# Optimization experiments

Measured on AMD Instinct MI355X. Metric: run time of the kernel, lower is better.

The kernel has to match this reference:

```python
import jax, jax.numpy as jnp
import numpy as np

B, S, E, H = 32, 2048, 256, 256

def setup_inputs() -> dict:
    key = jax.random.key(0)
    ks = jax.random.split(key, 8)
    scale = 1.0 / np.sqrt(H)  # kaiming-uniform-ish magnitude
    return {
        "x": jax.random.normal(ks[0], (B, S, E), dtype=jnp.float32),
        "h0": jax.random.normal(ks[1], (B, H), dtype=jnp.float32),
        "Wz": jax.random.normal(ks[2], (E, H), dtype=jnp.float32) * scale,
        "Uz": jax.random.normal(ks[3], (H, H), dtype=jnp.float32) * scale,
        "Wr": jax.random.normal(ks[4], (E, H), dtype=jnp.float32) * scale,
        "Ur": jax.random.normal(ks[5], (H, H), dtype=jnp.float32) * scale,
        "Wh": jax.random.normal(ks[6], (E, H), dtype=jnp.float32) * scale,
        "Uh": jax.random.normal(ks[7], (H, H), dtype=jnp.float32) * scale,
    }

def reference(x, h0, Wz, Uz, Wr, Ur, Wh, Uh):
    # Precompute input-side projections for all timesteps in three big GEMMs,
    # then scan the recurrence over time. Math identical to the per-step loop.
    xz = jnp.einsum('bse,eh->sbh', x, Wz)  # [S,B,H]
    xr = jnp.einsum('bse,eh->sbh', x, Wr)
    xh = jnp.einsum('bse,eh->sbh', x, Wh)

    def step(h, inp):
        xz_t, xr_t, xh_t = inp
        z = jax.nn.sigmoid(xz_t + h @ Uz)
        r = jax.nn.sigmoid(xr_t + h @ Ur)
        h_wave = jnp.tanh(xh_t + (r * h) @ Uh)
        h_new = (1.0 - z) * h + z * h_wave
        return h_new, h_new

    _, Ht = jax.lax.scan(step, h0, (xz, xr, xh))  # Ht: [S,B,H]
    return jnp.transpose(Ht, (1, 0, 2))  # [B,S,H]
```

## Files before the change

kernel.cpp:

```cpp
#include <hip/hip_runtime.h>

typedef _Float16 f16;
typedef _Float16 f16x2 __attribute__((ext_vector_type(2)));
typedef _Float16 f16x8 __attribute__((ext_vector_type(8)));
typedef __fp16   h16x2 __attribute__((ext_vector_type(2)));
typedef float    f32x4 __attribute__((ext_vector_type(4)));

#define B_ 32
#define S_ 2048
#define E_ 256
#define H_ 256
#define M_ (B_ * S_)

union U32F2 { unsigned int u; f16x2 h; h16x2 g; };

__device__ __forceinline__ float fdot2f(f16x2 a, f16x2 b, float c) {
#if __has_builtin(__builtin_amdgcn_fdot2)
  return __builtin_amdgcn_fdot2(a, b, c, false);
#else
  return c + (float)a.x * (float)b.x + (float)a.y * (float)b.y;
#endif
}

__device__ __forceinline__ float fast_exp2(float x) {
#if __has_builtin(__builtin_amdgcn_exp2f)
  return __builtin_amdgcn_exp2f(x);
#else
  return exp2f(x);
#endif
}
__device__ __forceinline__ float fast_rcp(float x) {
#if __has_builtin(__builtin_amdgcn_rcpf)
  return __builtin_amdgcn_rcpf(x);
#else
  return 1.0f / x;
#endif
}

__device__ __forceinline__ float sigm(float x) {
  float e = fast_exp2(-1.4426950408889634f * x);
  return fast_rcp(1.0f + e);
}
__device__ __forceinline__ float tanh_fast(float x) {
  x = fminf(15.0f, fmaxf(-15.0f, x));
  float e = fast_exp2(2.8853900817779268f * x);
  return (e - 1.0f) * fast_rcp(e + 1.0f);
}

__global__ __launch_bounds__(256, 4) void proj_gemm(
    const float* __restrict__ x, const float* __restrict__ Wz,
    const float* __restrict__ Wr, const float* __restrict__ Wh,
    f16* __restrict__ Xg) {
  __shared__ __align__(16) f16 Wl[64][264];
  const int tid = threadIdx.x;
  const int wv = tid >> 6;
  const int ln = tid & 63;
  const int M0 = blockIdx.x * 64;
  const int nb = blockIdx.y;
  const int gate = nb >> 2;
  const int c0 = (nb & 3) * 64;
  const float* W = (gate == 0) ? Wz : (gate == 1 ? Wr : Wh);

#pragma unroll
  for (int i = 0; i < 64; ++i) {
    int e = i * 256 + tid;
    int cl = e & 63;
    int k = e >> 6;
    Wl[cl][k] = (f16)W[(size_t)k * H_ + c0 + cl];
  }
  __syncthreads();

  const int row = M0 + wv * 16 + (ln & 15);
  const int kg = (ln >> 4) * 8;
  f32x4 acc0 = {0.f, 0.f, 0.f, 0.f};
  f32x4 acc1 = {0.f, 0.f, 0.f, 0.f};
  f32x4 acc2 = {0.f, 0.f, 0.f, 0.f};
  f32x4 acc3 = {0.f, 0.f, 0.f, 0.f};

#pragma unroll
  for (int kk = 0; kk < 8; ++kk) {
    const int k0 = kk * 32;
    const float* ap = x + (size_t)row * E_ + k0 + kg;
    float4 a0 = *(const float4*)ap;
    float4 a1 = *(const float4*)(ap + 4);
    f16x8 af = {(f16)a0.x, (f16)a0.y, (f16)a0.z, (f16)a0.w,
                (f16)a1.x, (f16)a1.y, (f16)a1.z, (f16)a1.w};
    f16x8 b0 = *(const f16x8*)&Wl[0 * 16 + (ln & 15)][k0 + kg];
    f16x8 b1 = *(const f16x8*)&Wl[1 * 16 + (ln & 15)][k0 + kg];
    f16x8 b2 = *(const f16x8*)&Wl[2 * 16 + (ln & 15)][k0 + kg];
    f16x8 b3 = *(const f16x8*)&Wl[3 * 16 + (ln & 15)][k0 + kg];
    acc0 = __builtin_amdgcn_mfma_f32_16x16x32_f16(af, b0, acc0, 0, 0, 0);
    acc1 = __builtin_amdgcn_mfma_f32_16x16x32_f16(af, b1, acc1, 0, 0, 0);
    acc2 = __builtin_amdgcn_mfma_f32_16x16x32_f16(af, b2, acc2, 0, 0, 0);
    acc3 = __builtin_amdgcn_mfma_f32_16x16x32_f16(af, b3, acc3, 0, 0, 0);
  }

  f16* outg = Xg + (size_t)gate * ((size_t)M_ * H_);
  const int rbase = M0 + wv * 16 + (ln >> 4) * 4;
#define EPI(NT, ACC)                                                       \
  {                                                                        \
    const int cc = c0 + NT * 16 + (ln & 15);                               \
    outg[(size_t)(rbase + 0) * H_ + cc] = (f16)ACC[0];                     \
    outg[(size_t)(rbase + 1) * H_ + cc] = (f16)ACC[1];                     \
    outg[(size_t)(rbase + 2) * H_ + cc] = (f16)ACC[2];                     \
    outg[(size_t)(rbase + 3) * H_ + cc] = (f16)ACC[3];                     \
  }
  EPI(0, acc0) EPI(1, acc1) EPI(2, acc2) EPI(3, acc3)
#undef EPI
}

__global__ __launch_bounds__(512, 2) void gru_rec(
    const f16* __restrict__ Xg, const float* __restrict__ h0,
    const float* __restrict__ Uz, const float* __restrict__ Ur,
    const float* __restrict__ Uh, float* __restrict__ out) {
  __shared__ uint4 h2v[32];
  __shared__ uint4 rh2v[32];
  const int b = blockIdx.x;
  const int tid = threadIdx.x;
  const int wv = tid >> 6;
  const int ln = tid & 63;
  const int c = wv * 32 + (ln & 31);
  const int hi = ln >> 5;
  const bool owner = (hi == 0);

  f16x2 wz[64], wr[64], wh[64];
  {
    const int rb = hi * 128;
#pragma unroll
    for (int j = 0; j < 64; ++j) {
      const size_t o0 = (size_t)(rb + 2 * j) * H_ + c;
      const size_t o1 = o0 + H_;
      wz[j] = f16x2{(f16)Uz[o0], (f16)Uz[o1]};
      wr[j] = f16x2{(f16)Ur[o0], (f16)Ur[o1]};
      wh[j] = f16x2{(f16)Uh[o0], (f16)Uh[o1]};
    }
  }

  float h_reg = 0.f;
  if (owner) h_reg = h0[b * H_ + c];
  {
    float hn = __shfl_xor(h_reg, 1);
    if (owner && !(ln & 1)) {
      U32F2 p; p.g = __builtin_amdgcn_cvt_pkrtz(h_reg, hn);
      ((unsigned int*)h2v)[c >> 1] = p.u;
    }
  }
  __syncthreads();

  const f16* xz = Xg + (size_t)b * ((size_t)S_ * H_) + c;
  const f16* xr = xz + (size_t)M_ * H_;
  const f16* xh = xr + (size_t)M_ * H_;
  float* outp = out + (size_t)b * ((size_t)S_ * H_) + c;

  f16 pz = xz[0], pr = xr[0], ph = xh[0];

  for (int t = 0; t < S_; ++t) {
    const float xzc = (float)pz, xrc = (float)pr, xhc = (float)ph;
    {
      const int t2 = (t + 1 < S_) ? (t + 1) : t;
      const size_t off = (size_t)t2 * H_;
      pz = xz[off]; pr = xr[off]; ph = xh[off];
    }

    float az = 0.f, ar = 0.f;
#pragma unroll
    for (int q = 0; q < 16; ++q) {
      uint4 hv = h2v[hi * 16 + q];
      U32F2 p0, p1, p2, p3;
      p0.u = hv.x; p1.u = hv.y; p2.u = hv.z; p3.u = hv.w;
      az = fdot2f(wz[4 * q + 0], p0.h, az);
      az = fdot2f(wz[4 * q + 1], p1.h, az);
      az = fdot2f(wz[4 * q + 2], p2.h, az);
      az = fdot2f(wz[4 * q + 3], p3.h, az);
      ar = fdot2f(wr[4 * q + 0], p0.h, ar);
      ar = fdot2f(wr[4 * q + 1], p1.h, ar);
      ar = fdot2f(wr[4 * q + 2], p2.h, ar);
      ar = fdot2f(wr[4 * q + 3], p3.h, ar);
    }
    az += __shfl_xor(az, 32);
    ar += __shfl_xor(ar, 32);

    float z_s = 0.f, rh = 0.f;
    if (owner) {
      z_s = sigm(az + xzc);
      float rr = sigm(ar + xrc);
      rh = rr * h_reg;
    }
    {
      float rhn = __shfl_xor(rh, 1);
      if (owner && !(ln & 1)) {
        U32F2 p; p.g = __builtin_amdgcn_cvt_pkrtz(rh, rhn);
        ((unsigned int*)rh2v)[c >> 1] = p.u;
      }
    }
    __syncthreads();

    float ah = 0.f;
#pragma unroll
    for (int q = 0; q < 16; ++q) {
      uint4 rv = rh2v[hi * 16 + q];
      U32F2 p0, p1, p2, p3;
      p0.u = rv.x; p1.u = rv.y; p2.u = rv.z; p3.u = rv.w;
      ah = fdot2f(wh[4 * q + 0], p0.h, ah);
      ah = fdot2f(wh[4 * q + 1], p1.h, ah);
      ah = fdot2f(wh[4 * q + 2], p2.h, ah);
      ah = fdot2f(wh[4 * q + 3], p3.h, ah);
    }
    ah += __shfl_xor(ah, 32);

    if (owner) {
      float ht = tanh_fast(ah + xhc);
      h_reg = h_reg + z_s * (ht - h_reg);
      outp[(size_t)t * H_] = h_reg;
    }
    {
      float hn = __shfl_xor(h_reg, 1);
      if (owner && !(ln & 1)) {
        U32F2 p; p.g = __builtin_amdgcn_cvt_pkrtz(h_reg, hn);
        ((unsigned int*)h2v)[c >> 1] = p.u;
      }
    }
    __syncthreads();
  }
}

extern "C" void kernel_launch(void* const* d_in, const int* in_sizes, int n_in,
                              void* d_out, int out_size, void* d_ws,
                              size_t ws_size, hipStream_t stream) {
  const float* x  = (const float*)d_in[0];
  const float* h0 = (const float*)d_in[1];
  const float* Wz = (const float*)d_in[2];
  const float* Uz = (const float*)d_in[3];
  const float* Wr = (const float*)d_in[4];
  const float* Ur = (const float*)d_in[5];
  const float* Wh = (const float*)d_in[6];
  const float* Uh = (const float*)d_in[7];
  float* out = (float*)d_out;

  const size_t need = (size_t)3 * M_ * H_ * sizeof(f16);
  if (ws_size < need) return;
  f16* Xg = (f16*)d_ws;

  proj_gemm<<<dim3(M_ / 64, 12), 256, 0, stream>>>(x, Wz, Wr, Wh, Xg);
  gru_rec<<<dim3(B_), 512, 0, stream>>>(Xg, h0, Uz, Ur, Uh, out);
}
```

Baseline: 2.967 ms.

## Split GRU recurrence K-dimension four ways across 1024-thread blocks

The recurrent kernel now uses 1024 threads per batch row. Each column's 256-long dot product is split across four 16-lane groups instead of two 32-lane halves, which halves the serial fdot2 chain per step and the weight registers per thread. The shared hidden-state vectors are padded per quarter so the four groups read from different banks. The Uh dot product is split into two accumulators for more ILP. In exchange, each step pays an extra cross-lane reduction, and each barrier now synchronises 16 waves instead of 8.

After: 3.633 ms. +22.4%, slower.

```diff
diff --git a/kernel.cpp b/kernel.cpp
--- a/kernel.cpp
+++ b/kernel.cpp
@@ -21,6 +21,10 @@
   return c + (float)a.x * (float)b.x + (float)a.y * (float)b.y;
 #endif
 }
+__device__ __forceinline__ float fdot2u(unsigned int w, unsigned int v, float c) {
+  U32F2 a, b; a.u = w; b.u = v;
+  return fdot2f(a.h, b.h, c);
+}
 
 __device__ __forceinline__ float fast_exp2(float x) {
 #if __has_builtin(__builtin_amdgcn_exp2f)
@@ -36,7 +40,6 @@
   return 1.0f / x;
 #endif
 }
-
 __device__ __forceinline__ float sigm(float x) {
   float e = fast_exp2(-1.4426950408889634f * x);
   return fast_rcp(1.0f + e);
@@ -109,31 +112,38 @@
 #undef EPI
 }
 
-__global__ __launch_bounds__(512, 2) void gru_rec(
+__global__ __launch_bounds__(1024) void gru_rec(
     const f16* __restrict__ Xg, const float* __restrict__ h0,
     const float* __restrict__ Uz, const float* __restrict__ Ur,
     const float* __restrict__ Uh, float* __restrict__ out) {
-  __shared__ uint4 h2v[32];
-  __shared__ uint4 rh2v[32];
+  __shared__ __align__(16) unsigned int h2v[4 * 36];
+  __shared__ __align__(16) unsigned int rh2v[4 * 36];
   const int b = blockIdx.x;
   const int tid = threadIdx.x;
   const int wv = tid >> 6;
   const int ln = tid & 63;
-  const int c = wv * 32 + (ln & 31);
-  const int hi = ln >> 5;
-  const bool owner = (hi == 0);
-
-  f16x2 wz[64], wr[64], wh[64];
+  const int c = wv * 16 + (ln & 15);
+  const int kq = ln >> 4;
+  const bool owner = (kq == 0);
+
+  unsigned int wzU[32], wrU[32], whU[32];
   {
-    const int rb = hi * 128;
-#pragma unroll
-    for (int j = 0; j < 64; ++j) {
+    const int rb = kq * 64;
+#pragma unroll
+    for (int j = 0; j < 32; ++j) {
       const size_t o0 = (size_t)(rb + 2 * j) * H_ + c;
-      const size_t o1 = o0 + H_;
-      wz[j] = f16x2{(f16)Uz[o0], (f16)Uz[o1]};
-      wr[j] = f16x2{(f16)Ur[o0], (f16)Ur[o1]};
-      wh[j] = f16x2{(f16)Uh[o0], (f16)Uh[o1]};
-    }
+      U32F2 pz, pr, ph;
+      pz.h = f16x2{(f16)Uz[o0], (f16)Uz[o0 + H_]};
+      pr.h = f16x2{(f16)Ur[o0], (f16)Ur[o0 + H_]};
+      ph.h = f16x2{(f16)Uh[o0], (f16)Uh[o0 + H_]};
+      wzU[j] = pz.u; wrU[j] = pr.u; whU[j] = ph.u;
+    }
+  }
+#pragma unroll
+  for (int j = 0; j < 32; ++j) {
+    asm("" : "+v"(wzU[j]));
+    asm("" : "+v"(wrU[j]));
+    asm("" : "+v"(whU[j]));
   }
 
   float h_reg = 0.f;
@@ -142,7 +152,8 @@
     float hn = __shfl_xor(h_reg, 1);
     if (owner && !(ln & 1)) {
       U32F2 p; p.g = __builtin_amdgcn_cvt_pkrtz(h_reg, hn);
-      ((unsigned int*)h2v)[c >> 1] = p.u;
+      const int pi = c >> 1;
+      h2v[(pi >> 5) * 36 + (pi & 31)] = p.u;
     }
   }
   __syncthreads();
@@ -153,6 +164,9 @@
   float* outp = out + (size_t)b * ((size_t)S_ * H_) + c;
 
   f16 pz = xz[0], pr = xr[0], ph = xh[0];
+
+  const uint4* hq = (const uint4*)(h2v + kq * 36);
+  const uint4* rq = (const uint4*)(rh2v + kq * 36);
 
   for (int t = 0; t < S_; ++t) {
     const float xzc = (float)pz, xrc = (float)pr, xhc = (float)ph;
@@ -164,21 +178,19 @@
 
     float az = 0.f, ar = 0.f;
 #pragma unroll
-    for (int q = 0; q < 16; ++q) {
-      uint4 hv = h2v[hi * 16 + q];
-      U32F2 p0, p1, p2, p3;
-      p0.u = hv.x; p1.u = hv.y; p2.u = hv.z; p3.u = hv.w;
-      az = fdot2f(wz[4 * q + 0], p0.h, az);
-      az = fdot2f(wz[4 * q + 1], p1.h, az);
-      az = fdot2f(wz[4 * q + 2], p2.h, az);
-      az = fdot2f(wz[4 * q + 3], p3.h, az);
-      ar = fdot2f(wr[4 * q + 0], p0.h, ar);
-      ar = fdot2f(wr[4 * q + 1], p1.h, ar);
-      ar = fdot2f(wr[4 * q + 2], p2.h, ar);
-      ar = fdot2f(wr[4 * q + 3], p3.h, ar);
-    }
-    az += __shfl_xor(az, 32);
-    ar += __shfl_xor(ar, 32);
+    for (int i = 0; i < 8; ++i) {
+      uint4 hv = hq[i];
+      az = fdot2u(wzU[4 * i + 0], hv.x, az);
+      az = fdot2u(wzU[4 * i + 1], hv.y, az);
+      az = fdot2u(wzU[4 * i + 2], hv.z, az);
+      az = fdot2u(wzU[4 * i + 3], hv.w, az);
+      ar = fdot2u(wrU[4 * i + 0], hv.x, ar);
+      ar = fdot2u(wrU[4 * i + 1], hv.y, ar);
+      ar = fdot2u(wrU[4 * i + 2], hv.z, ar);
+      ar = fdot2u(wrU[4 * i + 3], hv.w, ar);
+    }
+    az += __shfl_xor(az, 16); az += __shfl_xor(az, 32);
+    ar += __shfl_xor(ar, 16); ar += __shfl_xor(ar, 32);
 
     float z_s = 0.f, rh = 0.f;
     if (owner) {
@@ -190,23 +202,23 @@
       float rhn = __shfl_xor(rh, 1);
       if (owner && !(ln & 1)) {
         U32F2 p; p.g = __builtin_amdgcn_cvt_pkrtz(rh, rhn);
-        ((unsigned int*)rh2v)[c >> 1] = p.u;
+        const int pi = c >> 1;
+        rh2v[(pi >> 5) * 36 + (pi & 31)] = p.u;
       }
     }
     __syncthreads();
 
-    float ah = 0.f;
-#pragma unroll
-    for (int q = 0; q < 16; ++q) {
-      uint4 rv = rh2v[hi * 16 + q];
-      U32F2 p0, p1, p2, p3;
-      p0.u = rv.x; p1.u = rv.y; p2.u = rv.z; p3.u = rv.w;
-      ah = fdot2f(wh[4 * q + 0], p0.h, ah);
-      ah = fdot2f(wh[4 * q + 1], p1.h, ah);
-      ah = fdot2f(wh[4 * q + 2], p2.h, ah);
-      ah = fdot2f(wh[4 * q + 3], p3.h, ah);
-    }
-    ah += __shfl_xor(ah, 32);
+    float ah0 = 0.f, ah1 = 0.f;
+#pragma unroll
+    for (int i = 0; i < 8; ++i) {
+      uint4 rv = rq[i];
+      ah0 = fdot2u(whU[4 * i + 0], rv.x, ah0);
+      ah1 = fdot2u(whU[4 * i + 1], rv.y, ah1);
+      ah0 = fdot2u(whU[4 * i + 2], rv.z, ah0);
+      ah1 = fdot2u(whU[4 * i + 3], rv.w, ah1);
+    }
+    float ah = ah0 + ah1;
+    ah += __shfl_xor(ah, 16); ah += __shfl_xor(ah, 32);
 
     if (owner) {
       float ht = tanh_fast(ah + xhc);
@@ -217,7 +229,8 @@
       float hn = __shfl_xor(h_reg, 1);
       if (owner && !(ln & 1)) {
         U32F2 p; p.g = __builtin_amdgcn_cvt_pkrtz(h_reg, hn);
-        ((unsigned int*)h2v)[c >> 1] = p.u;
+        const int pi = c >> 1;
+        h2v[(pi >> 5) * 36 + (pi & 31)] = p.u;
       }
     }
     __syncthreads();
@@ -242,5 +255,5 @@
   f16* Xg = (f16*)d_ws;
 
   proj_gemm<<<dim3(M_ / 64, 12), 256, 0, stream>>>(x, Wz, Wr, Wh, Xg);
-  gru_rec<<<dim3(B_), 512, 0, stream>>>(Xg, h0, Uz, Ur, Uh, out);
-}
+  gru_rec<<<dim3(B_), 1024, 0, stream>>>(Xg, h0, Uz, Ur, Uh, out);
+}
```
